# Kernel tuning notes

Hardware: AMD Instinct MI355X
Metric: run time of the kernel (lower is better)

The kernel has to match this reference:

```python
import jax, jax.numpy as jnp
import numpy as np

# Topology constants (size='medium')
N_SW = 131      # 49 + 32 + 24 + 16 + 10
N_L = 64        # n_wavelengths
N_M = 32        # n_modes
PS = 4          # patch_size
V1_START, V1_COUNT = 0, 49
OUT_START, OUT_COUNT = 121, 10
DECAY = 0.15


def _encode(images):
    # images: [B, 28, 28] -> patches [B, 49, 16] -> pad to n_modes -> [B, 49, 64, 32]
    B = images.shape[0]
    p = images[:, :28, :28].reshape(B, 7, PS, 7, PS)
    p = p.transpose(0, 1, 3, 2, 4).reshape(B, 49, PS * PS)
    p = jnp.pad(p, ((0, 0), (0, 0), (0, N_M - PS * PS)))
    w_idx = jnp.arange(N_L, dtype=jnp.float32)
    w_weights = 1.0 - jnp.abs(w_idx - 32.0) / 64.0
    return p[:, :, None, :] * w_weights[None, None, :, None]


def _phase_step(field_r, field_i, out_r, out_i, conn_r, conn_i, phase, gain_sp):
    # Complex gather over switch graph: contract source switch dim s against conn[s, t]
    g_r = jnp.einsum('bsLm,st->btLm', out_r, conn_r) - jnp.einsum('bsLm,st->btLm', out_i, conn_i)
    g_i = jnp.einsum('bsLm,st->btLm', out_r, conn_i) + jnp.einsum('bsLm,st->btLm', out_i, conn_r)
    cp = jnp.cos(phase)[None, :, None, None]
    sp = jnp.sin(phase)[None, :, None, None]
    gr = g_r * cp - g_i * sp
    gi = g_r * sp + g_i * cp
    field_r = field_r * (1.0 - DECAY) + gr * 0.25
    field_i = field_i * (1.0 - DECAY) + gi * 0.25
    mag = jnp.sqrt(field_r ** 2 + field_i ** 2 + 1e-8)
    new_mag = jnp.tanh(mag * gain_sp[None, :, None, None])
    scale = new_mag / (mag + 1e-8)
    return field_r, field_i, field_r * scale, field_i * scale


def setup_inputs() -> dict:
    key = jax.random.key(0)
    k_img, k_mag, k_ph, k_w = jax.random.split(key, 4)
    images = jax.random.normal(k_img, (128, 28, 28), dtype=jnp.float32)
    conn_mag = jnp.abs(jax.random.normal(k_mag, (N_SW, N_SW), dtype=jnp.float32)) * 0.03
    conn_phase = jax.random.normal(k_ph, (N_SW, N_SW), dtype=jnp.float32) * 0.1
    conn_real = conn_mag * jnp.cos(conn_phase)
    conn_imag = conn_mag * jnp.sin(conn_phase)
    switch_phase = jnp.zeros((N_SW,), dtype=jnp.float32)
    switch_gain = jnp.ones((N_SW,), dtype=jnp.float32)
    readout_w = jax.random.normal(k_w, (10, OUT_COUNT), dtype=jnp.float32) * 0.1
    readout_b = jnp.zeros((10,), dtype=jnp.float32)
    return {
        'images': images,
        'conn_real': conn_real,
        'conn_imag': conn_imag,
        'switch_phase': switch_phase,
        'switch_gain': switch_gain,
        'readout_w': readout_w,
        'readout_b': readout_b,
        'n_steps': 10,
        'injection_steps': 4,
    }


def reference(images, conn_real, conn_imag, switch_phase, switch_gain,
              readout_w, readout_b, n_steps, injection_steps):
    enc = _encode(images)
    enc_max = jnp.max(jnp.abs(enc))
    enc = enc * jnp.where(enc_max > 1e-8, 1.0 / enc_max, 1.0)
    B = images.shape[0]
    field_r = jnp.zeros((B, N_SW, N_L, N_M), dtype=images.dtype)
    field_i = jnp.zeros_like(field_r)
    out_r = jnp.zeros_like(field_r)
    out_i = jnp.zeros_like(field_r)
    gain_sp = jax.nn.softplus(switch_gain)
    inj = enc * 0.3  # [B, 49, 64, 32], goes into V1 slots
    for t in range(n_steps):
        if t < injection_steps:
            field_r = field_r.at[:, V1_START:V1_START + V1_COUNT].add(inj)
        field_r, field_i, out_r, out_i = _phase_step(
            field_r, field_i, out_r, out_i, conn_real, conn_imag, switch_phase, gain_sp)
    orr = out_r[:, OUT_START:OUT_START + OUT_COUNT]
    oii = out_i[:, OUT_START:OUT_START + OUT_COUNT]
    energy = (orr ** 2 + oii ** 2).sum(axis=(2, 3))
    features = jnp.log1p(energy + 1e-8)
    return features @ readout_w.T + readout_b
```

## Files before the change

kernel.cpp:

```cpp
#include <hip/hip_runtime.h>
#include <cmath>


#define NSTEPS  10
#define INJ_ST  4
#define MT      144
#define NTASK   4224

typedef __bf16 bf16x8 __attribute__((ext_vector_type(8)));
typedef __bf16 bf16x4 __attribute__((ext_vector_type(4)));
typedef short  short8 __attribute__((ext_vector_type(8)));
typedef float  f32x4  __attribute__((ext_vector_type(4)));

#define WS_ENERGY 64
#define WS_PMAX   1536
#define WS_GSP    2048
#define WS_CONN   4096

__global__ void k_pre(const float* __restrict__ img,
                      const float* __restrict__ cr, const float* __restrict__ ci,
                      const float* __restrict__ phase, const float* __restrict__ gain,
                      float* ws) {
    if (blockIdx.x < 64) {
        __shared__ float sm[256];
        float v = 0.f;
        for (int i = blockIdx.x * 256 + threadIdx.x; i < 128 * 28 * 28; i += 64 * 256)
            v = fmaxf(v, fabsf(img[i]));
        sm[threadIdx.x] = v;
        __syncthreads();
        for (int s = 128; s > 0; s >>= 1) {
            if (threadIdx.x < s) sm[threadIdx.x] = fmaxf(sm[threadIdx.x], sm[threadIdx.x + s]);
            __syncthreads();
        }
        if (threadIdx.x == 0) ws[WS_PMAX + blockIdx.x] = sm[0];
        return;
    }
    int i = (blockIdx.x - 64) * 256 + threadIdx.x;
    __bf16* Cb = (__bf16*)(ws + WS_CONN);
    const int NCE = MT * 160;
    if (i < NCE) {
        int m = i / 160, k = i % 160;
        float vr = 0.f, vi = 0.f;
        if (m < 131 && k < 131) {
            float a = cr[k * 131 + m], b = ci[k * 131 + m];
            float ph = phase[m];
            float cp = cosf(ph), sp = sinf(ph);
            vr = a * cp - b * sp;
            vi = a * sp + b * cp;
        }
        int ca = ((k >> 3) * MT + m) * 8 + (k & 7);
        Cb[ca]       = (__bf16)vr;
        Cb[NCE + ca] = (__bf16)vi;
    } else if (i < NCE + MT) {
        int j = i - NCE;
        float g = 0.f;
        if (j < 131) {
            float x = gain[j];
            g = (x > 20.f) ? x : log1pf(expf(x));
        }
        ws[WS_GSP + j] = g * -0.72134754543f;
    } else if (i < NCE + MT + 1280) {
        ws[WS_ENERGY + (i - NCE - MT)] = 0.f;
    }
}

static __device__ __forceinline__ f32x4 MF(bf16x8 a, bf16x8 b, f32x4 c) {
    return __builtin_amdgcn_mfma_f32_16x16x32_bf16(a, b, c, 0, 0, 0);
}
static __device__ __forceinline__ bf16x8 bneg(bf16x8 a) {
    short8 t = __builtin_bit_cast(short8, a) ^ (short8)(short)0x8000;
    return __builtin_bit_cast(bf16x8, t);
}

#define CPAIR(AR, AI, BR, BI, BNI, P)                                  \
    accr[P] = MF(AR, BR,  accr[P]);                                    \
    accr[P] = MF(AI, BNI, accr[P]);                                    \
    acci[P] = MF(AR, BI,  acci[P]);                                    \
    acci[P] = MF(AI, BR,  acci[P]);

__global__ __launch_bounds__(512, 2)
void k_main(const float* __restrict__ img, const float* __restrict__ ws,
            float* __restrict__ energy) {
    __shared__ __bf16 CrL[18 * MT * 8];
    __shared__ __bf16 CiL[18 * MT * 8];
    __shared__ __bf16 OBP[2][8][18 * 16 * 8];
    __shared__ float  gspL[144];

    const int tid  = threadIdx.x;
    const int lane = tid & 63;
    const int ln15 = lane & 15;
    const int quad = lane >> 4;
    const int w    = __builtin_amdgcn_readfirstlane(tid >> 6);

    __bf16* __restrict__ OWr = &OBP[0][w][0];
    __bf16* __restrict__ OWi = &OBP[1][w][0];

    float mx = 0.f;
#pragma unroll
    for (int q = 0; q < 64; ++q) mx = fmaxf(mx, ws[WS_PMAX + q]);
    const float sc = (mx > 1e-8f) ? (1.02f / mx) : 1.02f;

    {
        const int4* srcR = (const int4*)(ws + WS_CONN);
        const int4* srcI = (const int4*)(ws + WS_CONN + (MT * 160 / 2));
        int4* dstR = (int4*)CrL;
        int4* dstI = (int4*)CiL;
        for (int i = tid; i < 2592; i += 512) { dstR[i] = srcR[i]; dstI[i] = srcI[i]; }
        if (tid < 144) gspL[tid] = ws[WS_GSP + tid];
    }
    __syncthreads();

#pragma unroll 1
    for (int r = 0; r < 3; ++r) {
        int T;
        if (r < 2) {
            T = r * 2048 + blockIdx.x * 8 + w;
        } else {
            if (w != 0 || blockIdx.x >= 128) break;
            T = 4096 + blockIdx.x;
        }
        if (T >= NTASK) break;
        const int u  = T >> 7;
        const int im = T & 127;
        const float wl  = 1.0f - fabsf((float)u - 32.0f) * (1.0f / 64.0f);
        const float wgt = (u == 0 || u == 32) ? 1.0f : 2.0f;
        const int imgb = im * 784 + (ln15 >> 2) * 28 + (ln15 & 3);

        f32x4 accr[9], acci[9];
#pragma unroll
        for (int p = 0; p < 9; ++p) { accr[p] = (f32x4)0.f; acci[p] = (f32x4)0.f; }

        auto inj_add = [&]() {
#pragma unroll
            for (int mt = 0; mt < 4; ++mt) {
#pragma unroll
                for (int rr = 0; rr < 4; ++rr) {
                    int j = mt * 16 + quad * 4 + rr;
                    if (j < 49) {
                        int pi = j / 7, pj = j % 7;
                        float px = img[imgb + pi * 112 + pj * 4];
                        float t  = px * sc;
                        accr[mt][rr] = fmaf(t, wl, accr[mt][rr]);
                    }
                }
            }
        };

        auto epilogue = [&]() {
#pragma unroll
            for (int mt = 0; mt < 9; ++mt) {
                f32x4 g2v = *(const f32x4*)(gspL + mt * 16 + quad * 4);
                bf16x4 pr, pi;
#pragma unroll
                for (int rr = 0; rr < 4; ++rr) {
                    float ar = accr[mt][rr], ai = acci[mt][rr];
                    float mag2 = fmaf(ar, ar, fmaf(ai, ai, 1.6e-7f));
                    float rsq  = __builtin_amdgcn_rsqf(mag2);
                    float e    = __builtin_amdgcn_exp2f(g2v[rr] * (mag2 * rsq));
                    float uu   = __builtin_amdgcn_rcpf(1.0f + e);
                    float th   = fmaf(-2.0f, e * uu, 1.0f);
                    float scv  = th * rsq;
                    pr[rr] = (__bf16)(ar * scv); pi[rr] = (__bf16)(ai * scv);
                }
                const int off = ((mt * 2 + (quad >> 1)) * 16 + ln15) * 8
                              + (quad & 1) * 4;
                *(bf16x4*)(OWr + off) = pr;
                *(bf16x4*)(OWi + off) = pi;
            }
        };

        inj_add();
        epilogue();

#pragma unroll 1
        for (int t = 1; t < NSTEPS - 1; ++t) {
#pragma unroll
            for (int p = 0; p < 9; ++p) { accr[p] *= 0.85f; acci[p] *= 0.85f; }
            if (t < INJ_ST) inj_add();

            const int ktEnd = (t == 1) ? 2 : 5;
#pragma unroll 1
            for (int kt = 0; kt < ktEnd; ++kt) {
                const int kch = kt * 4 + quad;
                const int rk  = (kch > 17) ? 17 : kch;
                const int bb  = (rk * 16 + ln15) * 8;
                bf16x8 br = *(const bf16x8*)(OWr + bb);
                bf16x8 bi = *(const bf16x8*)(OWi + bb);
                const int ab = (rk * MT + ln15) * 8;
                bf16x8 ar[9], ai[9];
#pragma unroll
                for (int mt = 0; mt < 9; ++mt) {
                    ar[mt] = *(const bf16x8*)(CrL + ab + mt * 128);
                    ai[mt] = *(const bf16x8*)(CiL + ab + mt * 128);
                }
                bf16x8 bn = bneg(bi);
#pragma unroll
                for (int mt = 0; mt < 9; ++mt) {
                    CPAIR(ar[mt], ai[mt], br, bi, bn, mt)
                }
            }
            epilogue();
        }

        accr[7] *= 0.85f; acci[7] *= 0.85f;
        accr[8] *= 0.85f; acci[8] *= 0.85f;
#pragma unroll 1
        for (int kt = 0; kt < 5; ++kt) {
            const int kch = kt * 4 + quad;
            const int rk  = (kch > 17) ? 17 : kch;
            const int bb  = (rk * 16 + ln15) * 8;
            bf16x8 br = *(const bf16x8*)(OWr + bb);
            bf16x8 bi = *(const bf16x8*)(OWi + bb);
            const int ab = (rk * MT + ln15) * 8;
            bf16x8 ar7 = *(const bf16x8*)(CrL + ab + 7 * 128);
            bf16x8 ai7 = *(const bf16x8*)(CiL + ab + 7 * 128);
            bf16x8 ar8 = *(const bf16x8*)(CrL + ab + 8 * 128);
            bf16x8 ai8 = *(const bf16x8*)(CiL + ab + 8 * 128);
            bf16x8 bn = bneg(bi);
            CPAIR(ar7, ai7, br, bi, bn, 7)
            CPAIR(ar8, ai8, br, bi, bn, 8)
        }

#pragma unroll
        for (int mt = 7; mt < 9; ++mt) {
#pragma unroll
            for (int rr = 0; rr < 4; ++rr) {
                int j = mt * 16 + quad * 4 + rr;
                if (j >= 121 && j <= 130) {
                    float ar = accr[mt][rr], ai = acci[mt][rr];
                    float mag2 = fmaf(ar, ar, fmaf(ai, ai, 1.6e-7f));
                    float rsq  = __builtin_amdgcn_rsqf(mag2);
                    float e    = __builtin_amdgcn_exp2f(gspL[j] * (mag2 * rsq));
                    float uu   = __builtin_amdgcn_rcpf(1.0f + e);
                    float th   = fmaf(-2.0f, e * uu, 1.0f);
                    float scv  = th * rsq;
                    float orv = ar * scv, oiv = ai * scv;
                    float e2 = orv * orv + oiv * oiv;
                    e2 += __shfl_xor(e2, 1);
                    e2 += __shfl_xor(e2, 2);
                    e2 += __shfl_xor(e2, 4);
                    e2 += __shfl_xor(e2, 8);
                    if (ln15 == 0)
                        atomicAdd(energy + im * 10 + (j - 121), e2 * wgt);
                }
            }
        }
    }
}

__global__ void k_readout(const float* __restrict__ ws,
                          const float* __restrict__ W,
                          const float* __restrict__ bias,
                          float* __restrict__ out) {
    int i = blockIdx.x * 256 + threadIdx.x;
    if (i < 1280) {
        int b = i / 10, o = i % 10;
        float s = bias[o];
#pragma unroll
        for (int f = 0; f < 10; ++f) {
            float feat = log1pf(ws[WS_ENERGY + b * 10 + f] + 1e-8f);
            s = fmaf(feat, W[o * 10 + f], s);
        }
        out[i] = s;
    }
}

extern "C" void kernel_launch(void* const* d_in, const int* in_sizes, int n_in,
                              void* d_out, int out_size, void* d_ws, size_t ws_size,
                              hipStream_t stream) {
    const float* images = (const float*)d_in[0];
    const float* conn_r = (const float*)d_in[1];
    const float* conn_i = (const float*)d_in[2];
    const float* phase  = (const float*)d_in[3];
    const float* gain   = (const float*)d_in[4];
    const float* W      = (const float*)d_in[5];
    const float* bias   = (const float*)d_in[6];
    float* ws  = (float*)d_ws;
    float* out = (float*)d_out;

    hipLaunchKernelGGL(k_pre, dim3(160), dim3(256), 0, stream,
                       images, conn_r, conn_i, phase, gain, ws);
    hipLaunchKernelGGL(k_main, dim3(256), dim3(512), 0, stream,
                       images, ws, ws + WS_ENERGY);
    hipLaunchKernelGGL(k_readout, dim3(5), dim3(256), 0, stream, ws, W, bias, out);
}
```

Measured before the change: 188.1 us.

## Split tail wavelength tasks across all eight waves of the block

Before, the 128 leftover tasks (wavelength 32) ran on a single wave per block while the other seven waves sat idle, which made a long serial tail. Now each of the first 128 blocks processes one leftover task cooperatively: each wave owns one 16-row output tile, and the bf16 outputs are exchanged through shared memory with block barriers between steps. Only the waves owning the readout rows run the final step. This cuts the tail latency at the cost of extra __syncthreads and a new, hand-specialised code path.

```diff
diff --git a/kernel.cpp b/kernel.cpp
--- a/kernel.cpp
+++ b/kernel.cpp
@@ -111,15 +111,8 @@
     __syncthreads();
 
 #pragma unroll 1
-    for (int r = 0; r < 3; ++r) {
-        int T;
-        if (r < 2) {
-            T = r * 2048 + blockIdx.x * 8 + w;
-        } else {
-            if (w != 0 || blockIdx.x >= 128) break;
-            T = 4096 + blockIdx.x;
-        }
-        if (T >= NTASK) break;
+    for (int r = 0; r < 2; ++r) {
+        const int T  = r * 2048 + blockIdx.x * 8 + w;
         const int u  = T >> 7;
         const int im = T & 127;
         const float wl  = 1.0f - fabsf((float)u - 32.0f) * (1.0f / 64.0f);
@@ -246,6 +239,153 @@
             }
         }
     }
+
+    if (blockIdx.x < 128) {
+        __syncthreads();
+        const int im = blockIdx.x;
+        const float wl  = 1.0f;
+        const float wgt = 1.0f;
+        const int imgb = im * 784 + (ln15 >> 2) * 28 + (ln15 & 3);
+
+        __bf16* __restrict__ SOr = &OBP[0][0][0];
+        __bf16* __restrict__ SOi = &OBP[1][0][0];
+        const int  mt0  = w;
+        const bool has8 = (w == 0);
+
+        f32x4 accr[2], acci[2];
+        accr[0] = (f32x4)0.f; acci[0] = (f32x4)0.f;
+        accr[1] = (f32x4)0.f; acci[1] = (f32x4)0.f;
+
+        auto inj_one = [&]() {
+            if (mt0 < 4) {
+#pragma unroll
+                for (int rr = 0; rr < 4; ++rr) {
+                    int j = mt0 * 16 + quad * 4 + rr;
+                    if (j < 49) {
+                        int pi = j / 7, pj = j % 7;
+                        float px = img[imgb + pi * 112 + pj * 4];
+                        float t2 = px * sc;
+                        accr[0][rr] = fmaf(t2, wl, accr[0][rr]);
+                    }
+                }
+            }
+        };
+
+        auto epi_one = [&](int idx, int mt) {
+            f32x4 g2v = *(const f32x4*)(gspL + mt * 16 + quad * 4);
+            bf16x4 pr, pi;
+#pragma unroll
+            for (int rr = 0; rr < 4; ++rr) {
+                float ar = accr[idx][rr], ai = acci[idx][rr];
+                float mag2 = fmaf(ar, ar, fmaf(ai, ai, 1.6e-7f));
+                float rsq  = __builtin_amdgcn_rsqf(mag2);
+                float e    = __builtin_amdgcn_exp2f(g2v[rr] * (mag2 * rsq));
+                float uu   = __builtin_amdgcn_rcpf(1.0f + e);
+                float th   = fmaf(-2.0f, e * uu, 1.0f);
+                float scv  = th * rsq;
+                pr[rr] = (__bf16)(ar * scv); pi[rr] = (__bf16)(ai * scv);
+            }
+            const int off = ((mt * 2 + (quad >> 1)) * 16 + ln15) * 8
+                          + (quad & 1) * 4;
+            *(bf16x4*)(SOr + off) = pr;
+            *(bf16x4*)(SOi + off) = pi;
+        };
+
+        inj_one();
+        epi_one(0, mt0);
+        if (has8) epi_one(1, 8);
+        __syncthreads();
+
+#pragma unroll 1
+        for (int t = 1; t < NSTEPS - 1; ++t) {
+            accr[0] *= 0.85f; acci[0] *= 0.85f;
+            accr[1] *= 0.85f; acci[1] *= 0.85f;
+            if (t < INJ_ST) inj_one();
+
+            const int ktEnd = (t == 1) ? 2 : 5;
+#pragma unroll 1
+            for (int kt = 0; kt < ktEnd; ++kt) {
+                const int kch = kt * 4 + quad;
+                const int rk  = (kch > 17) ? 17 : kch;
+                const int bb  = (rk * 16 + ln15) * 8;
+                bf16x8 br = *(const bf16x8*)(SOr + bb);
+                bf16x8 bi = *(const bf16x8*)(SOi + bb);
+                const int ab = (rk * MT + ln15) * 8;
+                bf16x8 a0r = *(const bf16x8*)(CrL + ab + mt0 * 128);
+                bf16x8 a0i = *(const bf16x8*)(CiL + ab + mt0 * 128);
+                bf16x8 bn = bneg(bi);
+                accr[0] = MF(a0r, br, accr[0]);
+                accr[0] = MF(a0i, bn, accr[0]);
+                acci[0] = MF(a0r, bi, acci[0]);
+                acci[0] = MF(a0i, br, acci[0]);
+                if (has8) {
+                    bf16x8 a1r = *(const bf16x8*)(CrL + ab + 8 * 128);
+                    bf16x8 a1i = *(const bf16x8*)(CiL + ab + 8 * 128);
+                    accr[1] = MF(a1r, br, accr[1]);
+                    accr[1] = MF(a1i, bn, accr[1]);
+                    acci[1] = MF(a1r, bi, acci[1]);
+                    acci[1] = MF(a1i, br, acci[1]);
+                }
+            }
+            __syncthreads();
+            epi_one(0, mt0);
+            if (has8) epi_one(1, 8);
+            __syncthreads();
+        }
+
+        accr[0] *= 0.85f; acci[0] *= 0.85f;
+        accr[1] *= 0.85f; acci[1] *= 0.85f;
+        if (w == 7 || w == 0) {
+#pragma unroll 1
+            for (int kt = 0; kt < 5; ++kt) {
+                const int kch = kt * 4 + quad;
+                const int rk  = (kch > 17) ? 17 : kch;
+                const int bb  = (rk * 16 + ln15) * 8;
+                bf16x8 br = *(const bf16x8*)(SOr + bb);
+                bf16x8 bi = *(const bf16x8*)(SOi + bb);
+                const int ab = (rk * MT + ln15) * 8;
+                bf16x8 bn = bneg(bi);
+                if (w == 7) {
+                    bf16x8 a0r = *(const bf16x8*)(CrL + ab + 7 * 128);
+                    bf16x8 a0i = *(const bf16x8*)(CiL + ab + 7 * 128);
+                    accr[0] = MF(a0r, br, accr[0]);
+                    accr[0] = MF(a0i, bn, accr[0]);
+                    acci[0] = MF(a0r, bi, acci[0]);
+                    acci[0] = MF(a0i, br, acci[0]);
+                } else {
+                    bf16x8 a1r = *(const bf16x8*)(CrL + ab + 8 * 128);
+                    bf16x8 a1i = *(const bf16x8*)(CiL + ab + 8 * 128);
+                    accr[1] = MF(a1r, br, accr[1]);
+                    accr[1] = MF(a1i, bn, accr[1]);
+                    acci[1] = MF(a1r, bi, acci[1]);
+                    acci[1] = MF(a1i, br, acci[1]);
+                }
+            }
+            const int mtE  = (w == 7) ? 7 : 8;
+            const int idxE = (w == 7) ? 0 : 1;
+#pragma unroll
+            for (int rr = 0; rr < 4; ++rr) {
+                int j = mtE * 16 + quad * 4 + rr;
+                if (j >= 121 && j <= 130) {
+                    float ar = accr[idxE][rr], ai = acci[idxE][rr];
+                    float mag2 = fmaf(ar, ar, fmaf(ai, ai, 1.6e-7f));
+                    float rsq  = __builtin_amdgcn_rsqf(mag2);
+                    float e    = __builtin_amdgcn_exp2f(gspL[j] * (mag2 * rsq));
+                    float uu   = __builtin_amdgcn_rcpf(1.0f + e);
+                    float th   = fmaf(-2.0f, e * uu, 1.0f);
+                    float scv  = th * rsq;
+                    float orv = ar * scv, oiv = ai * scv;
+                    float e2 = orv * orv + oiv * oiv;
+                    e2 += __shfl_xor(e2, 1);
+                    e2 += __shfl_xor(e2, 2);
+                    e2 += __shfl_xor(e2, 4);
+                    e2 += __shfl_xor(e2, 8);
+                    if (ln15 == 0)
+                        atomicAdd(energy + im * 10 + (j - 121), e2 * wgt);
+                }
+            }
+        }
+    }
 }
 
 __global__ void k_readout(const float* __restrict__ ws,
```

After: 184.6 us. About the same (-1.8%).
